# Performance work log

Hardware: AMD Instinct MI355X
Metric: run time of the kernel (lower is better)

The kernel has to match this reference:

```python
import jax, jax.numpy as jnp
import numpy as np

H_DIM = 1024
N_HEADS = 16
HEAD_DIM = H_DIM // N_HEADS
MAX_POS = 2048   # RotaryEmbedding default max_position_embeddings
BASE = 10000.0
SCALING_FACTOR = 1.0


def rotate_half(x):
    # interleaved convention: cat([-x[..., 1::2], x[..., ::2]], -1)
    return jnp.concatenate([-x[..., 1::2], x[..., ::2]], axis=-1)


def rope_cos_sin(seq_len, dtype):
    # LlamaDynamicNTKScalingRotaryEmbedding._set_cos_sin_cache
    base = BASE
    if seq_len > MAX_POS:
        base = BASE * (SCALING_FACTOR * seq_len / MAX_POS - (SCALING_FACTOR - 1.0)) ** (HEAD_DIM / (HEAD_DIM - 2))
    inv_freq = 1.0 / (base ** (jnp.arange(0, HEAD_DIM, 2, dtype=jnp.float32) / HEAD_DIM))
    t = jnp.arange(seq_len, dtype=jnp.float32)
    freqs = jnp.einsum('i,j->ij', t, inv_freq)          # [S, D/2]
    emb = jnp.concatenate([freqs, freqs], axis=-1)       # [S, D]
    return emb.astype(dtype), jnp.cos(emb).astype(dtype), jnp.sin(emb).astype(dtype)


def setup_inputs() -> dict:
    key = jax.random.key(0)
    ks = jax.random.split(key, 5)
    B, S = 1, 4096
    scale_w = 0.02
    return {
        'hidden_states': jax.random.normal(ks[0], (B, S, H_DIM), dtype=jnp.float32),
        'Wq': jax.random.normal(ks[1], (H_DIM, H_DIM), dtype=jnp.float32) * scale_w,
        'Wk': jax.random.normal(ks[2], (H_DIM, H_DIM), dtype=jnp.float32) * scale_w,
        'Wv': jax.random.normal(ks[3], (H_DIM, H_DIM), dtype=jnp.float32) * scale_w,
        'Wo': jax.random.normal(ks[4], (H_DIM, H_DIM), dtype=jnp.float32) * scale_w,
    }


def reference(hidden_states, Wq, Wk, Wv, Wo):
    B, S, H = hidden_states.shape
    # projections (nn.Linear: x @ W.T)
    def proj(x, W):
        y = jnp.einsum('bsh,oh->bso', x, W)
        return y.reshape(B, S, N_HEADS, HEAD_DIM).transpose(0, 2, 1, 3)  # bhsd
    q = proj(hidden_states, Wq)
    k = proj(hidden_states, Wk)
    v = proj(hidden_states, Wv)

    _, cos, sin = rope_cos_sin(S, hidden_states.dtype)
    cos = cos[None, None, :, :]   # [1,1,S,D] (position_ids = arange(S)[None], unsqueeze(1))
    sin = sin[None, None, :, :]
    q = q * cos + rotate_half(q) * sin
    k = k * cos + rotate_half(k) * sin

    # NOTE: source DIVIDES by scale = head_dim**-0.5 (i.e. multiplies by sqrt(d))
    scale = HEAD_DIM ** (-0.5)
    attn = jnp.einsum('bhsd,bhtd->bhst', q, k) / scale
    attn = jax.nn.softmax(attn, axis=-1)
    out = jnp.einsum('bhst,bhtd->bhsd', attn, v)
    out = out.transpose(0, 2, 1, 3).reshape(B, S, H)
    return jnp.einsum('bsh,oh->bso', out, Wo)
```

## Files before the change

### kernel.cpp

```cpp
#include <hip/hip_runtime.h>
#include <cmath>
#include <cstdint>

#define S_LEN 4096
#define NH 16
#define HD 64

typedef _Float16 f16x8 __attribute__((ext_vector_type(8)));
typedef __attribute__((ext_vector_type(4))) float f32x4;
typedef __attribute__((ext_vector_type(16))) float f32x16;
typedef __attribute__((ext_vector_type(4))) unsigned short u16x4;
typedef __attribute__((ext_vector_type(4))) unsigned int u32x4;
typedef __attribute__((ext_vector_type(4))) float f4;

__device__ __forceinline__ unsigned short f2h(float x) {
  union { _Float16 h; unsigned short u; } v; v.h = (_Float16)x; return v.u;
}
__device__ __forceinline__ float h2f(unsigned short u) {
  union { unsigned short u; _Float16 h; } v; v.u = u; return (float)v.h;
}
__device__ __forceinline__ float permx32(float v) {
  int idx = (((int)(threadIdx.x & 63)) ^ 32) << 2;
  return __int_as_float(__builtin_amdgcn_ds_bpermute(idx, __float_as_int(v)));
}
__device__ __forceinline__ unsigned permx32u(unsigned v) {
  int idx = (((int)(threadIdx.x & 63)) ^ 32) << 2;
  return (unsigned)__builtin_amdgcn_ds_bpermute(idx, (int)v);
}
__device__ __forceinline__ float exp2a(float x) {
  float r; asm("v_exp_f32 %0, %1" : "=v"(r) : "v"(x)); return r;
}
__device__ __forceinline__ unsigned pkh(float a, float b) {
  unsigned r;
  asm("v_cvt_pkrtz_f16_f32 %0, %1, %2" : "=v"(r) : "v"(a), "v"(b));
  return r;
}

#define GLL16(g, l) __builtin_amdgcn_global_load_lds( \
    (const __attribute__((address_space(1))) void*)(g), \
    (__attribute__((address_space(3))) void*)(l), 16, 0, 0)

#define PLANE_BYTES 524288
#define TILE_BYTES 8192

__global__ __launch_bounds__(256) void cvt_kernel(
    const float* __restrict__ hs, const float* __restrict__ wq,
    const float* __restrict__ wk, const float* __restrict__ wv,
    const float* __restrict__ wo,
    unsigned short* __restrict__ hs16,
    unsigned short* __restrict__ wq16, unsigned short* __restrict__ wk16,
    unsigned short* __restrict__ wv16, unsigned short* __restrict__ wo16)
{
  const int HID4 = (S_LEN * 1024) / 4;
  const int W4   = (1024 * 1024) / 4;
  const int total = HID4 + 4 * W4;
  for (int i = blockIdx.x * 256 + threadIdx.x; i < total;
       i += gridDim.x * 256) {
    const float* s; unsigned short* d; int off;
    if (i < HID4) { s = hs; d = hs16; off = i; }
    else {
      int j = i - HID4; int w = j >> 18; off = j & (W4 - 1);
      s = (w == 0) ? wq : (w == 1) ? wk : (w == 2) ? wv : wo;
      d = (w == 0) ? wq16 : (w == 1) ? wk16 : (w == 2) ? wv16 : wo16;
    }
    f4 v = *(const f4*)(s + (size_t)off * 4);
    u16x4 r;
#pragma unroll
    for (int j = 0; j < 4; j++) r[j] = f2h(v[j]);
    *(u16x4*)(d + (size_t)off * 4) = r;
  }
}

__global__ __launch_bounds__(256) void rope_table(
    float* __restrict__ cosT, float* __restrict__ sinT, double base)
{
  int idx = blockIdx.x * 256 + threadIdx.x;
  if (idx >= S_LEN * 32) return;
  int t = idx >> 5, j = idx & 31;
  double invf = pow(base, -(double)j / 32.0);
  double f = fmod((double)t * invf, 6.283185307179586476925286766559);
  float ff = (float)f;
  cosT[idx] = cosf(ff);
  sinT[idx] = sinf(ff);
}

__global__ __launch_bounds__(256) void gemm_f16(
    const unsigned short* __restrict__ A,
    const unsigned short* __restrict__ B0, const unsigned short* __restrict__ B1,
    const unsigned short* __restrict__ B2,
    void* O0, void* O1, void* O2, int M, int K, int fin)
{
  __shared__ unsigned short As[128 * 64];
  __shared__ unsigned short Bs[128 * 64];
  const int z = blockIdx.z;
  const unsigned short* B = (z == 0) ? B0 : (z == 1) ? B1 : B2;
  void* O = (z == 0) ? O0 : (z == 1) ? O1 : O2;
  const int m0 = blockIdx.y * 128, n0 = blockIdx.x * 128;
  const int tid = threadIdx.x, wid = tid >> 6, lane = tid & 63;
  const int lr = lane & 15, lk = (lane >> 4) * 8;
  const int wr = (wid >> 1) * 64, wc = (wid & 1) * 64;
  const int strow = lane >> 3;
  const int stcol = (lane & 7) * 8;

  f32x4 acc[4][4];
#pragma unroll
  for (int m = 0; m < 4; m++)
#pragma unroll
    for (int n = 0; n < 4; n++) acc[m][n] = (f32x4){0.f, 0.f, 0.f, 0.f};

  for (int kt = 0; kt < K; kt += 64) {
#pragma unroll
    for (int i = 0; i < 4; i++) {
      int c = wid * 4 + i;
      int row = c * 8 + strow;
      GLL16(A + (size_t)(m0 + row) * K + kt + stcol, &As[c * 512]);
      GLL16(B + (size_t)(n0 + row) * K + kt + stcol, &Bs[c * 512]);
    }
    __syncthreads();
    f16x8 af[4][2], bfr[4][2];
#pragma unroll
    for (int m = 0; m < 4; m++)
#pragma unroll
      for (int kk = 0; kk < 2; kk++)
        af[m][kk] = *(const f16x8*)&As[(wr + m * 16 + lr) * 64 + kk * 32 + lk];
#pragma unroll
    for (int n = 0; n < 4; n++)
#pragma unroll
      for (int kk = 0; kk < 2; kk++)
        bfr[n][kk] = *(const f16x8*)&Bs[(wc + n * 16 + lr) * 64 + kk * 32 + lk];
#pragma unroll
    for (int m = 0; m < 4; m++)
#pragma unroll
      for (int n = 0; n < 4; n++)
#pragma unroll
        for (int kk = 0; kk < 2; kk++)
          acc[m][n] = __builtin_amdgcn_mfma_f32_16x16x32_f16(
              af[m][kk], bfr[n][kk], acc[m][n], 0, 0, 0);
    __syncthreads();
  }

  const int rbase = m0 + wr + (lane >> 4) * 4;
  const int cbase = n0 + wc + lr;
  if (fin) {
    float* C = (float*)O;
#pragma unroll
    for (int m = 0; m < 4; m++)
#pragma unroll
      for (int n = 0; n < 4; n++)
#pragma unroll
        for (int j = 0; j < 4; j++) {
          int s = rbase + m * 16 + j;
          int o = cbase + n * 16;
          C[(size_t)s * 1024 + o] = acc[m][n][j];
        }
  } else if (z == 2) {
    char* base = (char*)O;
#pragma unroll
    for (int m = 0; m < 4; m++)
#pragma unroll
      for (int n = 0; n < 4; n++) {
        int s = rbase + m * 16;
        int o = cbase + n * 16;
        int hd = o >> 6, d = o & 63;
        size_t tb = (size_t)hd * PLANE_BYTES + (size_t)(s >> 6) * TILE_BYTES
                  + (size_t)d * 128;
        int cbyte = (2 * (s & 63)) ^ ((d & 7) << 4);
        u16x4 r;
#pragma unroll
        for (int j = 0; j < 4; j++) r[j] = f2h(acc[m][n][j]);
        *(u16x4*)(base + tb + cbyte) = r;
      }
  } else {
    unsigned short* C = (unsigned short*)O;
#pragma unroll
    for (int m = 0; m < 4; m++)
#pragma unroll
      for (int n = 0; n < 4; n++)
#pragma unroll
        for (int j = 0; j < 4; j++) {
          int s = rbase + m * 16 + j;
          int o = cbase + n * 16;
          C[((size_t)(o >> 6) * M + s) * HD + (o & 63)] = f2h(acc[m][n][j]);
        }
  }
}

__global__ __launch_bounds__(256) void rope_apply(
    const unsigned short* __restrict__ Qh, const unsigned short* __restrict__ Kh,
    unsigned short* __restrict__ Q16, char* __restrict__ Kt,
    const float* __restrict__ cosT, const float* __restrict__ sinT)
{
  int wid = threadIdx.x >> 6, lane = threadIdx.x & 63;
  int row = blockIdx.x * 4 + wid;
  int t = row & (S_LEN - 1);
  int head = row >> 12;
  int j = (lane < 32) ? lane : (lane - 32);
  float c = cosT[t * 32 + j], s = sinT[t * 32 + j];
  int partner = (lane < 32) ? (2 * lane + 1) : (2 * (lane - 32));
  float sgn = (lane < 32) ? -1.0f : 1.0f;
  float q = h2f(Qh[(size_t)row * HD + lane]);
  float k = h2f(Kh[(size_t)row * HD + lane]);
  float qo = __shfl(q, partner, 64);
  float ko = __shfl(k, partner, 64);
  float qr = (q * c + sgn * qo * s) * 11.541560327111707f;
  float kr = k * c + sgn * ko * s;
  Q16[(size_t)row * HD + lane] = f2h(qr);
  size_t kb = (size_t)head * PLANE_BYTES + (size_t)(t >> 6) * TILE_BYTES
            + (size_t)(t & 63) * 128 + ((2 * lane) ^ ((t & 7) << 4));
  *(unsigned short*)(Kt + kb) = f2h(kr);
}

__global__ __launch_bounds__(256, 4) void attn_kernel(
    const unsigned short* __restrict__ Q16, const char* __restrict__ Kt,
    const char* __restrict__ Vt,
    unsigned short* __restrict__ Opart, float* __restrict__ Ml)
{
  __shared__ char KL[2][TILE_BYTES];
  __shared__ char VL[2][TILE_BYTES];

  const int tid = threadIdx.x, wid = tid >> 6, lane = tid & 63;
  const int l5 = lane & 31, hi2 = lane >> 5;
  const bool lohalf = (hi2 == 0);
  const int z = blockIdx.z;

  int id = blockIdx.x + 32 * blockIdx.y;
  int h  = (id & 7) + 8 * ((id >> 3) & 1);
  int bx = id >> 4;
  const int qw = bx * 128 + wid * 32;

  const size_t hoff = (size_t)h * PLANE_BYTES;
  const char* KtH = Kt + hoff;
  const char* VtH = Vt + hoff;

  const unsigned short* Qrow = Q16 + ((size_t)h * S_LEN + qw + l5) * HD;
  f16x8 qf[4];
#pragma unroll
  for (int ks = 0; ks < 4; ks++)
    qf[ks] = *(const f16x8*)&Qrow[ks * 16 + hi2 * 8];

  f32x16 o0 = (f32x16)0.0f, o1 = (f32x16)0.0f;
  float m_q = -__builtin_inff(), l_q = 0.f;

  const int T0 = z * 32;
  const int NT = 32;

#define STAGE(kt, b) do { \
    size_t tb = (size_t)(T0 + (kt)) * TILE_BYTES; \
    _Pragma("unroll") \
    for (int c = 0; c < 2; c++) { \
      int ub = c * 4096 + wid * 1024; \
      int go = ub + lane * 16; \
      GLL16(KtH + tb + go, &KL[b][ub]); \
      GLL16(VtH + tb + go, &VL[b][ub]); \
    } } while (0)

  STAGE(0, 0);

  for (int kt = 0; kt < NT; ++kt) {
    const int cur = kt & 1;
    asm volatile("s_waitcnt vmcnt(0)" ::: "memory");
    __builtin_amdgcn_s_barrier();
    asm volatile("" ::: "memory");

    if (kt + 1 < NT) STAGE(kt + 1, cur ^ 1);

    f32x16 s0 = (f32x16)0.0f, s1 = (f32x16)0.0f;
    __builtin_amdgcn_s_setprio(1);
#pragma unroll
    for (int ks = 0; ks < 4; ks++) {
      const int coff = (32 * ks + 16 * hi2) ^ ((l5 & 7) << 4);
      f16x8 k0 = *(const f16x8*)(&KL[cur][l5 * 128 + coff]);
      f16x8 k1 = *(const f16x8*)(&KL[cur][(32 + l5) * 128 + coff]);
      s0 = __builtin_amdgcn_mfma_f32_32x32x16_f16(k0, qf[ks], s0, 0, 0, 0);
      s1 = __builtin_amdgcn_mfma_f32_32x32x16_f16(k1, qf[ks], s1, 0, 0, 0);
    }
    __builtin_amdgcn_s_setprio(0);

    float mx = fmaxf(s0[0], s1[0]);
#pragma unroll
    for (int r = 1; r < 16; r++) mx = fmaxf(mx, fmaxf(s0[r], s1[r]));
    mx = fmaxf(mx, permx32(mx));

    if (__any(mx > m_q + 11.0f)) {
      float mnew = fmaxf(m_q, mx);
      float alpha = exp2a(m_q - mnew);
      m_q = mnew;
      l_q *= alpha;
#pragma unroll
      for (int i = 0; i < 16; i++) { o0[i] *= alpha; o1[i] *= alpha; }
    }

    f16x8 pf[4];
    float rs = 0.f;
#pragma unroll
    for (int ks = 0; ks < 4; ks++) {
      f32x16 sv = (ks < 2) ? s0 : s1;
      const int base = (ks & 1) * 8;
      float e0 = exp2a(sv[base + 0] - m_q);
      float e1 = exp2a(sv[base + 1] - m_q);
      float e2 = exp2a(sv[base + 2] - m_q);
      float e3 = exp2a(sv[base + 3] - m_q);
      float e4 = exp2a(sv[base + 4] - m_q);
      float e5 = exp2a(sv[base + 5] - m_q);
      float e6 = exp2a(sv[base + 6] - m_q);
      float e7 = exp2a(sv[base + 7] - m_q);
      rs += ((e0 + e1) + (e2 + e3)) + ((e4 + e5) + (e6 + e7));
      unsigned a0 = pkh(e0, e1);
      unsigned a1 = pkh(e2, e3);
      unsigned b0 = pkh(e4, e5);
      unsigned b1 = pkh(e6, e7);
      unsigned sw0 = permx32u(lohalf ? b0 : a0);
      unsigned sw1 = permx32u(lohalf ? b1 : a1);
      u32x4 w;
      w[0] = lohalf ? a0 : sw0;
      w[1] = lohalf ? a1 : sw1;
      w[2] = lohalf ? sw0 : b0;
      w[3] = lohalf ? sw1 : b1;
      union { u32x4 u; f16x8 f; } cv; cv.u = w;
      pf[ks] = cv.f;
    }
    rs += permx32(rs);
    l_q += rs;

    __builtin_amdgcn_s_setprio(1);
#pragma unroll
    for (int ks = 0; ks < 4; ks++) {
      const int coff = (32 * ks + 16 * hi2) ^ ((l5 & 7) << 4);
      f16x8 v0 = *(const f16x8*)(&VL[cur][l5 * 128 + coff]);
      f16x8 v1 = *(const f16x8*)(&VL[cur][(32 + l5) * 128 + coff]);
      o0 = __builtin_amdgcn_mfma_f32_32x32x16_f16(v0, pf[ks], o0, 0, 0, 0);
      o1 = __builtin_amdgcn_mfma_f32_32x32x16_f16(v1, pf[ks], o1, 0, 0, 0);
    }
    __builtin_amdgcn_s_setprio(0);
  }
#undef STAGE

  const float inv = 1.0f / l_q;
  const int q = qw + l5;
  unsigned* orow = (unsigned*)(Opart + (((size_t)(z * NH + h)) * S_LEN + q) * HD);
#pragma unroll
  for (int k = 0; k < 8; k++) {
    const int d0 = 2 * (k & 1) + 8 * (k >> 1) + 4 * hi2;
    orow[d0 >> 1]        = pkh(o0[2 * k] * inv, o0[2 * k + 1] * inv);
    orow[(d0 + 32) >> 1] = pkh(o1[2 * k] * inv, o1[2 * k + 1] * inv);
  }
  if (hi2 == 0) {
    float2* mlp = (float2*)Ml + ((size_t)(z * NH + h)) * S_LEN + q;
    *mlp = make_float2(m_q, l_q);
  }
}

__global__ __launch_bounds__(256) void combine_kernel(
    const unsigned short* __restrict__ Opart, const float* __restrict__ Ml,
    unsigned short* __restrict__ Ab)
{
  const int NQ = S_LEN * 1024 / 4;
  for (int idx = blockIdx.x * 256 + threadIdx.x; idx < NQ;
       idx += gridDim.x * 256) {
    int e = idx * 4;
    int s = e >> 10;
    int col = e & 1023;
    int h = col >> 6, d = col & 63;
    const float2* mlb = (const float2*)Ml;
    float2 ml0 = mlb[(size_t)h * S_LEN + s];
    float2 ml1 = mlb[(size_t)(NH + h) * S_LEN + s];
    float mmax = fmaxf(ml0.x, ml1.x);
    float w0 = exp2f(ml0.x - mmax) * ml0.y;
    float w1 = exp2f(ml1.x - mmax) * ml1.y;
    float rden = 1.0f / (w0 + w1);
    float c0 = w0 * rden, c1 = w1 * rden;
    const unsigned short* p0 = Opart + ((size_t)h * S_LEN + s) * HD + d;
    const unsigned short* p1 = Opart + ((size_t)(NH + h) * S_LEN + s) * HD + d;
    u16x4 a = *(const u16x4*)p0;
    u16x4 b = *(const u16x4*)p1;
    u16x4 r;
#pragma unroll
    for (int j = 0; j < 4; j++)
      r[j] = f2h(c0 * h2f(a[j]) + c1 * h2f(b[j]));
    *(u16x4*)(Ab + e) = r;
  }
}

extern "C" void kernel_launch(void* const* d_in, const int* in_sizes, int n_in,
                              void* d_out, int out_size, void* d_ws, size_t ws_size,
                              hipStream_t stream)
{
  const float* hs = (const float*)d_in[0];
  const float* Wq = (const float*)d_in[1];
  const float* Wk = (const float*)d_in[2];
  const float* Wv = (const float*)d_in[3];
  const float* Wo = (const float*)d_in[4];

  char* ws = (char*)d_ws;
  const size_t HS = (size_t)S_LEN * 1024;
  const size_t WN = (size_t)1024 * 1024;
  size_t off = 0;
  unsigned short* hs16 = (unsigned short*)(ws + off); off += HS * 2;
  unsigned short* wq16 = (unsigned short*)(ws + off); off += WN * 2;
  unsigned short* wk16 = (unsigned short*)(ws + off); off += WN * 2;
  unsigned short* wv16 = (unsigned short*)(ws + off); off += WN * 2;
  unsigned short* wo16 = (unsigned short*)(ws + off); off += WN * 2;
  unsigned short* Qh16 = (unsigned short*)(ws + off); off += HS * 2;
  unsigned short* Kh16 = (unsigned short*)(ws + off); off += HS * 2;
  char* Kt_g = ws + off; off += (size_t)NH * PLANE_BYTES;
  char* VT_g = ws + off; off += (size_t)NH * PLANE_BYTES;
  unsigned short* Ab = (unsigned short*)(ws + off); off += HS * 2;
  float* Ml = (float*)(ws + off); off += (size_t)2 * NH * S_LEN * 8;
  float* cosT = (float*)(ws + off); off += (size_t)S_LEN * 32 * 4;
  float* sinT = (float*)(ws + off); off += (size_t)S_LEN * 32 * 4;
  unsigned short* Q16 = hs16;
  unsigned short* Opart = Qh16;

  cvt_kernel<<<4096, 256, 0, stream>>>(hs, Wq, Wk, Wv, Wo,
                                       hs16, wq16, wk16, wv16, wo16);

  double base = 10000.0 * pow((double)S_LEN / 2048.0, 64.0 / 62.0);
  rope_table<<<(S_LEN * 32 + 255) / 256, 256, 0, stream>>>(cosT, sinT, base);

  gemm_f16<<<dim3(8, 32, 3), 256, 0, stream>>>(
      hs16, wq16, wk16, wv16, Qh16, Kh16, VT_g, S_LEN, 1024, 0);

  rope_apply<<<NH * S_LEN / 4, 256, 0, stream>>>(
      Qh16, Kh16, Q16, Kt_g, cosT, sinT);

  attn_kernel<<<dim3(32, 16, 2), 256, 0, stream>>>(
      Q16, Kt_g, VT_g, Opart, Ml);

  combine_kernel<<<2048, 256, 0, stream>>>(Opart, Ml, Ab);

  gemm_f16<<<dim3(8, 32, 1), 256, 0, stream>>>(
      Ab, wo16, wo16, wo16, d_out, d_out, d_out, S_LEN, 1024, 1);
}
```

Measured before the change: 209.4 us.

## Software-pipeline attention QK^T with softmax, use permlane32_swap and max3, fuse rope table

```diff
diff --git a/kernel.cpp b/kernel.cpp
--- a/kernel.cpp
+++ b/kernel.cpp
@@ -11,6 +11,7 @@
 typedef __attribute__((ext_vector_type(16))) float f32x16;
 typedef __attribute__((ext_vector_type(4))) unsigned short u16x4;
 typedef __attribute__((ext_vector_type(4))) unsigned int u32x4;
+typedef int i32x2 __attribute__((ext_vector_type(2)));
 typedef __attribute__((ext_vector_type(4))) float f4;
 
 __device__ __forceinline__ unsigned short f2h(float x) {
@@ -22,10 +23,6 @@
 __device__ __forceinline__ float permx32(float v) {
   int idx = (((int)(threadIdx.x & 63)) ^ 32) << 2;
   return __int_as_float(__builtin_amdgcn_ds_bpermute(idx, __float_as_int(v)));
-}
-__device__ __forceinline__ unsigned permx32u(unsigned v) {
-  int idx = (((int)(threadIdx.x & 63)) ^ 32) << 2;
-  return (unsigned)__builtin_amdgcn_ds_bpermute(idx, (int)v);
 }
 __device__ __forceinline__ float exp2a(float x) {
   float r; asm("v_exp_f32 %0, %1" : "=v"(r) : "v"(x)); return r;
@@ -35,6 +32,11 @@
   asm("v_cvt_pkrtz_f16_f32 %0, %1, %2" : "=v"(r) : "v"(a), "v"(b));
   return r;
 }
+__device__ __forceinline__ float max3a(float a, float b, float c) {
+  float r;
+  asm("v_max3_f32 %0, %1, %2, %3" : "=v"(r) : "v"(a), "v"(b), "v"(c));
+  return r;
+}
 
 #define GLL16(g, l) __builtin_amdgcn_global_load_lds( \
     (const __attribute__((address_space(1))) void*)(g), \
@@ -43,19 +45,31 @@
 #define PLANE_BYTES 524288
 #define TILE_BYTES 8192
 
-__global__ __launch_bounds__(256) void cvt_kernel(
+__global__ __launch_bounds__(256) void cvt_table_kernel(
     const float* __restrict__ hs, const float* __restrict__ wq,
     const float* __restrict__ wk, const float* __restrict__ wv,
     const float* __restrict__ wo,
     unsigned short* __restrict__ hs16,
     unsigned short* __restrict__ wq16, unsigned short* __restrict__ wk16,
-    unsigned short* __restrict__ wv16, unsigned short* __restrict__ wo16)
-{
+    unsigned short* __restrict__ wv16, unsigned short* __restrict__ wo16,
+    float* __restrict__ cosT, float* __restrict__ sinT, double base)
+{
+  if (blockIdx.x >= 4096) {
+    int idx = (blockIdx.x - 4096) * 256 + threadIdx.x;
+    if (idx < S_LEN * 32) {
+      int t = idx >> 5, j = idx & 31;
+      double invf = pow(base, -(double)j / 32.0);
+      double f = fmod((double)t * invf, 6.283185307179586476925286766559);
+      float ff = (float)f;
+      cosT[idx] = cosf(ff);
+      sinT[idx] = sinf(ff);
+    }
+    return;
+  }
   const int HID4 = (S_LEN * 1024) / 4;
   const int W4   = (1024 * 1024) / 4;
   const int total = HID4 + 4 * W4;
-  for (int i = blockIdx.x * 256 + threadIdx.x; i < total;
-       i += gridDim.x * 256) {
+  for (int i = blockIdx.x * 256 + threadIdx.x; i < total; i += 4096 * 256) {
     const float* s; unsigned short* d; int off;
     if (i < HID4) { s = hs; d = hs16; off = i; }
     else {
@@ -69,19 +83,6 @@
     for (int j = 0; j < 4; j++) r[j] = f2h(v[j]);
     *(u16x4*)(d + (size_t)off * 4) = r;
   }
-}
-
-__global__ __launch_bounds__(256) void rope_table(
-    float* __restrict__ cosT, float* __restrict__ sinT, double base)
-{
-  int idx = blockIdx.x * 256 + threadIdx.x;
-  if (idx >= S_LEN * 32) return;
-  int t = idx >> 5, j = idx & 31;
-  double invf = pow(base, -(double)j / 32.0);
-  double f = fmod((double)t * invf, 6.283185307179586476925286766559);
-  float ff = (float)f;
-  cosT[idx] = cosf(ff);
-  sinT[idx] = sinf(ff);
 }
 
 __global__ __launch_bounds__(256) void gemm_f16(
@@ -220,7 +221,6 @@
 
   const int tid = threadIdx.x, wid = tid >> 6, lane = tid & 63;
   const int l5 = lane & 31, hi2 = lane >> 5;
-  const bool lohalf = (hi2 == 0);
   const int z = blockIdx.z;
 
   int id = blockIdx.x + 32 * blockIdx.y;
@@ -254,31 +254,48 @@
       GLL16(VtH + tb + go, &VL[b][ub]); \
     } } while (0)
 
+#define QKT(b) do { \
+    s0 = (f32x16)0.0f; s1 = (f32x16)0.0f; \
+    __builtin_amdgcn_s_setprio(1); \
+    _Pragma("unroll") \
+    for (int ks = 0; ks < 4; ks++) { \
+      const int coff = (32 * ks + 16 * hi2) ^ ((l5 & 7) << 4); \
+      f16x8 k0 = *(const f16x8*)(&KL[b][l5 * 128 + coff]); \
+      f16x8 k1 = *(const f16x8*)(&KL[b][(32 + l5) * 128 + coff]); \
+      s0 = __builtin_amdgcn_mfma_f32_32x32x16_f16(k0, qf[ks], s0, 0, 0, 0); \
+      s1 = __builtin_amdgcn_mfma_f32_32x32x16_f16(k1, qf[ks], s1, 0, 0, 0); \
+    } \
+    __builtin_amdgcn_s_setprio(0); \
+  } while (0)
+
   STAGE(0, 0);
+  asm volatile("s_waitcnt vmcnt(0)" ::: "memory");
+  __builtin_amdgcn_s_barrier();
+  asm volatile("" ::: "memory");
+  STAGE(1, 1);
+
+  f32x16 s0, s1;
+  QKT(0);
 
   for (int kt = 0; kt < NT; ++kt) {
     const int cur = kt & 1;
-    asm volatile("s_waitcnt vmcnt(0)" ::: "memory");
-    __builtin_amdgcn_s_barrier();
-    asm volatile("" ::: "memory");
-
-    if (kt + 1 < NT) STAGE(kt + 1, cur ^ 1);
-
-    f32x16 s0 = (f32x16)0.0f, s1 = (f32x16)0.0f;
-    __builtin_amdgcn_s_setprio(1);
-#pragma unroll
-    for (int ks = 0; ks < 4; ks++) {
-      const int coff = (32 * ks + 16 * hi2) ^ ((l5 & 7) << 4);
-      f16x8 k0 = *(const f16x8*)(&KL[cur][l5 * 128 + coff]);
-      f16x8 k1 = *(const f16x8*)(&KL[cur][(32 + l5) * 128 + coff]);
-      s0 = __builtin_amdgcn_mfma_f32_32x32x16_f16(k0, qf[ks], s0, 0, 0, 0);
-      s1 = __builtin_amdgcn_mfma_f32_32x32x16_f16(k1, qf[ks], s1, 0, 0, 0);
-    }
-    __builtin_amdgcn_s_setprio(0);
-
-    float mx = fmaxf(s0[0], s1[0]);
-#pragma unroll
-    for (int r = 1; r < 16; r++) mx = fmaxf(mx, fmaxf(s0[r], s1[r]));
+
+    float t0 = max3a(s0[0],  s0[1],  s0[2]);
+    float t1 = max3a(s0[3],  s0[4],  s0[5]);
+    float t2 = max3a(s0[6],  s0[7],  s0[8]);
+    float t3 = max3a(s0[9],  s0[10], s0[11]);
+    float t4 = max3a(s0[12], s0[13], s0[14]);
+    float t5 = max3a(s0[15], s1[0],  s1[1]);
+    float t6 = max3a(s1[2],  s1[3],  s1[4]);
+    float t7 = max3a(s1[5],  s1[6],  s1[7]);
+    float t8 = max3a(s1[8],  s1[9],  s1[10]);
+    float t9 = max3a(s1[11], s1[12], s1[13]);
+    float ta = fmaxf(s1[14], s1[15]);
+    float u0 = max3a(t0, t1, t2);
+    float u1 = max3a(t3, t4, t5);
+    float u2 = max3a(t6, t7, t8);
+    float u3 = fmaxf(t9, ta);
+    float mx = fmaxf(max3a(u0, u1, u2), u3);
     mx = fmaxf(mx, permx32(mx));
 
     if (__any(mx > m_q + 11.0f)) {
@@ -291,7 +308,7 @@
     }
 
     f16x8 pf[4];
-    float rs = 0.f;
+    float g[4];
 #pragma unroll
     for (int ks = 0; ks < 4; ks++) {
       f32x16 sv = (ks < 2) ? s0 : s1;
@@ -304,23 +321,31 @@
       float e5 = exp2a(sv[base + 5] - m_q);
       float e6 = exp2a(sv[base + 6] - m_q);
       float e7 = exp2a(sv[base + 7] - m_q);
-      rs += ((e0 + e1) + (e2 + e3)) + ((e4 + e5) + (e6 + e7));
+      g[ks] = ((e0 + e1) + (e2 + e3)) + ((e4 + e5) + (e6 + e7));
       unsigned a0 = pkh(e0, e1);
       unsigned a1 = pkh(e2, e3);
       unsigned b0 = pkh(e4, e5);
       unsigned b1 = pkh(e6, e7);
-      unsigned sw0 = permx32u(lohalf ? b0 : a0);
-      unsigned sw1 = permx32u(lohalf ? b1 : a1);
+      i32x2 r0 = __builtin_amdgcn_permlane32_swap((int)a0, (int)b0, false, false);
+      i32x2 r1 = __builtin_amdgcn_permlane32_swap((int)a1, (int)b1, false, false);
       u32x4 w;
-      w[0] = lohalf ? a0 : sw0;
-      w[1] = lohalf ? a1 : sw1;
-      w[2] = lohalf ? sw0 : b0;
-      w[3] = lohalf ? sw1 : b1;
+      w[0] = (unsigned)r0[0];
+      w[1] = (unsigned)r1[0];
+      w[2] = (unsigned)r0[1];
+      w[3] = (unsigned)r1[1];
       union { u32x4 u; f16x8 f; } cv; cv.u = w;
       pf[ks] = cv.f;
     }
+    float rs = (g[0] + g[1]) + (g[2] + g[3]);
     rs += permx32(rs);
     l_q += rs;
+
+    if (kt + 1 < NT) {
+      asm volatile("s_waitcnt vmcnt(0)" ::: "memory");
+      __builtin_amdgcn_s_barrier();
+      asm volatile("" ::: "memory");
+      QKT(cur ^ 1);
+    }
 
     __builtin_amdgcn_s_setprio(1);
 #pragma unroll
@@ -332,8 +357,14 @@
       o1 = __builtin_amdgcn_mfma_f32_32x32x16_f16(v1, pf[ks], o1, 0, 0, 0);
     }
     __builtin_amdgcn_s_setprio(0);
+
+    asm volatile("" ::: "memory");
+    __builtin_amdgcn_s_barrier();
+    asm volatile("" ::: "memory");
+    if (kt + 2 < NT) STAGE(kt + 2, cur);
   }
 #undef STAGE
+#undef QKT
 
   const float inv = 1.0f / l_q;
   const int q = qw + l5;
@@ -411,11 +442,11 @@
   unsigned short* Q16 = hs16;
   unsigned short* Opart = Qh16;
 
-  cvt_kernel<<<4096, 256, 0, stream>>>(hs, Wq, Wk, Wv, Wo,
-                                       hs16, wq16, wk16, wv16, wo16);
-
   double base = 10000.0 * pow((double)S_LEN / 2048.0, 64.0 / 62.0);
-  rope_table<<<(S_LEN * 32 + 255) / 256, 256, 0, stream>>>(cosT, sinT, base);
+
+  cvt_table_kernel<<<4608, 256, 0, stream>>>(hs, Wq, Wk, Wv, Wo,
+                                             hs16, wq16, wk16, wv16, wo16,
+                                             cosT, sinT, base);
 
   gemm_f16<<<dim3(8, 32, 3), 256, 0, stream>>>(
       hs16, wq16, wk16, wv16, Qh16, Kh16, VT_g, S_LEN, 1024, 0);
```

After: 200.4 us. -4.3%, faster.
